# Optimization experiments

Measured on AMD Instinct MI355X. Metric: run time of the kernel, lower is better.

The kernel has to match this reference:

```python
import jax, jax.numpy as jnp
import numpy as np
from jax import lax

# ---- config (matches init_kwargs / detectron2-style inference defaults) ----
B, R, K = 8, 2000, 80          # images, proposals per image, foreground classes
H, W = 800.0, 1333.0           # image (height, width) used for box clipping
SCORE_THRESH = 0.05
NMS_THRESH = 0.5
M = 2048                        # fixed NMS candidate budget (pre-NMS top_k)
T = 100                         # topk_per_image


def setup_inputs() -> dict:
    key = jax.random.key(0)
    k1, k2, k3, k4, k5 = jax.random.split(key, 5)
    # well-formed proposal boxes (x1, y1, x2, y2)
    cx = jax.random.uniform(k1, (B, R)) * W
    cy = jax.random.uniform(k2, (B, R)) * H
    bw = jax.random.uniform(k3, (B, R)) * 300.0 + 2.0
    bh = jax.random.uniform(k4, (B, R)) * 300.0 + 2.0
    boxes = jnp.stack([cx - bw / 2, cy - bh / 2, cx + bw / 2, cy + bh / 2], axis=-1)
    k5a, k5b = jax.random.split(k5)
    scores = jax.random.uniform(k5a, (B, R, K + 1))          # (R, K+1), last col = bg
    bases = jax.random.normal(k5b, (B, R, 7)) * 0.1          # 6 base deltas + 1 h delta
    return {"boxes": boxes.astype(jnp.float32),
            "scores": scores.astype(jnp.float32),
            "bases": bases.astype(jnp.float32)}


def _delta_to_bases(bs, bx):
    # bs: (T, 6) deltas, bx: (T, 4) boxes -> (T, 10) polygon + midpoint
    firstx, firsty = bs[:, 2], bs[:, 3]
    secondx, secondy = bs[:, 4], bs[:, 5]
    x1, y1, x2, y2 = bx[:, 0], bx[:, 1], bx[:, 2], bx[:, 3]
    dx = x2 - x1
    dy = y2 - y1
    midx = (x1 + x2) / 2 + bs[:, 0] * dx
    midy = (y1 + y2) / 2 + bs[:, 1] * dy
    px1 = midx + firstx * dx
    py1 = midy + firsty * dy
    px2 = midx + secondx * dx
    py2 = midy + secondy * dy
    px3 = midx - secondx * dx
    py3 = midy - secondy * dy
    px4 = midx - firstx * dx
    py4 = midy - firsty * dy
    return jnp.stack((px1, py1, px2, py2, px3, py3, px4, py4, midx, midy), axis=-1)


def _delta_to_h(dh, bx):
    dy = bx[:, 3] - bx[:, 1]
    return dy + dh * dy


def _pairwise_iou(b):
    # b: (M, 4). Only used inside a boolean comparison -> no grad path, as in torch NMS.
    x1, y1, x2, y2 = b[:, 0], b[:, 1], b[:, 2], b[:, 3]
    area = jnp.clip(x2 - x1, 0) * jnp.clip(y2 - y1, 0)
    xx1 = jnp.maximum(x1[:, None], x1[None, :])
    yy1 = jnp.maximum(y1[:, None], y1[None, :])
    xx2 = jnp.minimum(x2[:, None], x2[None, :])
    yy2 = jnp.minimum(y2[:, None], y2[None, :])
    inter = jnp.clip(xx2 - xx1, 0) * jnp.clip(yy2 - yy1, 0)
    return inter / (area[:, None] + area[None, :] - inter + 1e-7)


def _single_image(boxes, scores, bases):
    finite = jnp.all(jnp.isfinite(boxes), axis=1) & jnp.all(jnp.isfinite(scores), axis=1)
    scores_k = scores[:, :-1]                                 # drop background (R,K)
    # Boxes.clip(image_shape)
    boxes = jnp.stack([jnp.clip(boxes[:, 0], 0.0, W),
                       jnp.clip(boxes[:, 1], 0.0, H),
                       jnp.clip(boxes[:, 2], 0.0, W),
                       jnp.clip(boxes[:, 3], 0.0, H)], axis=-1)
    # score threshold -> flat (R*K) candidate list, fixed-size top_k selection
    flat = jnp.where(finite[:, None] & (scores_k > SCORE_THRESH), scores_k, -jnp.inf)
    top_scores, top_idx = lax.top_k(flat.reshape(R * K), M)   # (M,)
    box_idx = top_idx // K
    cls = top_idx % K
    cboxes = boxes[box_idx]                                   # (M,4)
    cbases = bases[box_idx]                                   # (M,7)
    valid = jnp.isfinite(top_scores)
    # batched_nms: offset boxes per class so cross-class IoU = 0
    off = (cls.astype(boxes.dtype) * (jnp.maximum(H, W) + 2.0))[:, None]
    iou = _pairwise_iou(cboxes + off)                         # (M,M)

    def body(i, st):
        keep, supp = st
        ki = valid[i] & jnp.logical_not(supp[i])
        keep = keep.at[i].set(ki)
        supp = supp | (ki & (iou[i] > NMS_THRESH))
        return keep, supp

    keep, _ = lax.fori_loop(0, M, body,
                            (jnp.zeros((M,), bool), jnp.zeros((M,), bool)))
    masked = jnp.where(keep, top_scores, -jnp.inf)
    fscores, sel = lax.top_k(masked, T)                       # keep[:topk_per_image]
    fvalid = jnp.isfinite(fscores)
    fscores = jnp.where(fvalid, fscores, 0.0)
    fboxes = cboxes[sel] * fvalid[:, None]
    fbases = cbases[sel]
    fcls = jnp.where(fvalid, cls[sel], -1)
    h = _delta_to_h(fbases[:, 6], fboxes) * fvalid            # (T,)
    dec = _delta_to_bases(fbases[:, 0:6], fboxes) * fvalid[:, None]  # (T,10)
    return dec, h, fboxes, fscores, fcls, fvalid


def reference(boxes, scores, bases):
    # returns per-image padded detections:
    # pred_bases (B,T,10), pred_h (B,T), pred_boxes (B,T,4), scores (B,T),
    # pred_classes (B,T) int, valid mask (B,T)
    return jax.vmap(_single_image)(boxes, scores, bases)
```

## Files before the change

kernel.cpp:

```cpp
#include <hip/hip_runtime.h>
#include <stdint.h>

using u64 = unsigned long long;
using u32 = unsigned;

namespace {
constexpr int RR = 2000;
constexpr int KK = 80;
constexpr int KS = 81;
constexpr int BB = 8;
constexpr int MM = 2048;
constexpr int TT = 100;
constexpr int NB = 2048;
constexpr int CAP = 4096;
constexpr int SPLIT = 50;
constexpr int RPB = RR / SPLIT;
constexpr int FPB = RPB * KS;
constexpr int V4  = FPB / 4;
constexpr int CPB = RPB * KK;
constexpr int SPLIT_H = 10;
constexpr int RPB_H = RR / SPLIT_H;
constexpr int FPB_H = RPB_H * KS;
constexpr int V4_H  = FPB_H / 4;
constexpr float WW  = 1333.0f;
constexpr float HH  = 800.0f;
constexpr float OFF = 1335.0f;
constexpr float STH = 0.05f;
constexpr float NMS = 0.5f;

constexpr size_t HIST_OFF   = 0;
constexpr size_t CNT_OFF    = 65536;
constexpr size_t ZERO_BYTES = 65568;
constexpr size_t CSTAR_OFF  = 65568;
constexpr size_t ROWOK_OFF  = 65664;
constexpr size_t CAND_OFF   = 81920;
}

__global__ __launch_bounds__(1024) void k_hist(const float* __restrict__ boxes,
                                               const float* __restrict__ scores,
                                               u32* __restrict__ hist_g,
                                               unsigned char* __restrict__ rowok_g) {
    const int b = blockIdx.x / SPLIT_H, sb = blockIdx.x % SPLIT_H, tid = threadIdx.x;
    const int r0 = sb * RPB_H;
    const float4* sv = (const float4*)(scores + (size_t)b * RR * KS + (size_t)r0 * KS);
    __shared__ u32 bad[RPB_H];
    __shared__ u32 h[NB];

    const int q0 = tid, q1 = tid + 1024, q2 = tid + 2048, q3 = tid + 3072;
    const float4 v0 = sv[q0];
    const float4 v1 = sv[q1];
    const float4 v2 = sv[q2];
    const float4 v3 = (q3 < V4_H) ? sv[q3] : make_float4(0.f, 0.f, 0.f, 0.f);

    if (tid < RPB_H) bad[tid] = 0;
    for (int i = tid; i < NB; i += 1024) h[i] = 0;
    __syncthreads();

    if (tid < RPB_H) {
        const float4 bx = ((const float4*)(boxes + (size_t)b * RR * 4))[r0 + tid];
        if (!(isfinite(bx.x) && isfinite(bx.y) && isfinite(bx.z) && isfinite(bx.w)))
            atomicOr(&bad[tid], 1u);
    }
    auto chk = [&](int q, const float4& v) {
        if (q < V4_H) {
            const int i0 = 4 * q;
            if (!isfinite(v.x)) atomicOr(&bad[(i0    ) / KS], 1u);
            if (!isfinite(v.y)) atomicOr(&bad[(i0 + 1) / KS], 1u);
            if (!isfinite(v.z)) atomicOr(&bad[(i0 + 2) / KS], 1u);
            if (!isfinite(v.w)) atomicOr(&bad[(i0 + 3) / KS], 1u);
        }
    };
    chk(q0, v0); chk(q1, v1); chk(q2, v2); chk(q3, v3);
    __syncthreads();
    if (tid < RPB_H) rowok_g[b * RR + r0 + tid] = bad[tid] ? 0 : 1;

    auto acc = [&](int idx, float s) {
        const int r_l = idx / KS, k = idx - r_l * KS;
        if (k < KK && bad[r_l] == 0 && s > STH) {
            int bk = (int)(s * (float)NB);
            bk = min(max(bk, 0), NB - 1);
            atomicAdd(&h[bk], 1u);
        }
    };
    auto accv = [&](int q, const float4& v) {
        if (q < V4_H) {
            const int i0 = 4 * q;
            acc(i0, v.x); acc(i0 + 1, v.y); acc(i0 + 2, v.z); acc(i0 + 3, v.w);
        }
    };
    accv(q0, v0); accv(q1, v1); accv(q2, v2); accv(q3, v3);
    __syncthreads();
    for (int i = tid; i < NB; i += 1024)
        if (h[i]) atomicAdd(&hist_g[b * NB + i], h[i]);
}

__global__ __launch_bounds__(256) void k_cut(const u32* __restrict__ hist_g,
                                             u32* __restrict__ cstar_g) {
    const int b = blockIdx.x, tid = threadIdx.x;
    __shared__ u32 h[NB];
    __shared__ u32 cs[256];
    __shared__ u32 cstar_s;
    for (int i = tid; i < NB; i += 256) h[i] = hist_g[b * NB + i];
    if (tid == 0) cstar_s = 0;
    __syncthreads();

    u32 loc[8];
    const int hi = NB - 1 - 8 * tid;
    u32 sum = 0;
#pragma unroll
    for (int j = 0; j < 8; ++j) { loc[j] = h[hi - j]; sum += loc[j]; }
    cs[tid] = sum;
    __syncthreads();
    for (int s = 1; s < 256; s <<= 1) {
        const u32 t = (tid >= s) ? cs[tid - s] : 0u;
        __syncthreads();
        cs[tid] += t;
        __syncthreads();
    }
    const u32 P = cs[tid], Pm1 = (tid > 0) ? cs[tid - 1] : 0u;
    if (P >= (u32)MM && Pm1 < (u32)MM) {
        u32 run = Pm1;
#pragma unroll
        for (int j = 0; j < 8; ++j) {
            run += loc[j];
            if (run >= (u32)MM) { cstar_s = (u32)(hi - j); break; }
        }
    }
    __syncthreads();
    if (tid == 0) cstar_g[b] = cstar_s;
}

__global__ __launch_bounds__(256) void k_compact(const float* __restrict__ scores,
                                                 const u32* __restrict__ cstar_g,
                                                 const unsigned char* __restrict__ rowok_g,
                                                 u64* __restrict__ cand,
                                                 u32* __restrict__ cnt_g) {
    const int b = blockIdx.x / SPLIT, sb = blockIdx.x % SPLIT, tid = threadIdx.x;
    const int r0 = sb * RPB;
    const float4* sv = (const float4*)(scores + (size_t)b * RR * KS + (size_t)r0 * KS);
    __shared__ u64 stage[CPB];
    __shared__ u32 rok[RPB];
    __shared__ u32 scnt, base_s;
    if (tid < RPB) rok[tid] = rowok_g[b * RR + r0 + tid];
    if (tid == 0) scnt = 0;
    __syncthreads();
    const u32 cstar = cstar_g[b];

    auto put = [&](int idx, float s) {
        const int r_l = idx / KS, k = idx - r_l * KS;
        if (k < KK && rok[r_l] && s > STH) {
            int bk = (int)(s * (float)NB);
            bk = min(max(bk, 0), NB - 1);
            if ((u32)bk >= cstar) {
                const u32 p = atomicAdd(&scnt, 1u);
                const u32 eg = (u32)((r0 + r_l) * KK + k);
                stage[p] = ((u64)__float_as_uint(s) << 32) | (u32)(~eg);
            }
        }
    };
#pragma unroll
    for (int it = 0; it < 4; ++it) {
        const int q = tid + it * 256;
        if (q < V4) {
            const float4 v = sv[q];
            const int i0 = 4 * q;
            put(i0, v.x); put(i0 + 1, v.y); put(i0 + 2, v.z); put(i0 + 3, v.w);
        }
    }
    __syncthreads();
    if (tid == 0) base_s = atomicAdd(&cnt_g[b], scnt);
    __syncthreads();
    const u32 base = base_s, nn = scnt;
    u64* cb = cand + (size_t)b * CAP;
    for (u32 i = tid; i < nn; i += 256) {
        const u32 pos = base + i;
        if (pos < (u32)CAP) cb[pos] = stage[i];
    }
}

__device__ __forceinline__ void cmpsw(u64& a, u64& b, bool desc) {
    const u64 mx = a > b ? a : b, mn = a > b ? b : a;
    a = desc ? mx : mn;
    b = desc ? mn : mx;
}
template <unsigned KQ, unsigned JQ>
__device__ __forceinline__ void shfl_stage(u64 (&val)[4], int lane) {
#pragma unroll
    for (int r = 0; r < 4; ++r) {
        const unsigned v = (unsigned)(r * 64 + lane);
        const u64 pv = __shfl_xor(val[r], (int)JQ, 64);
        const bool keepmax = (((v & KQ) == 0) == (((unsigned)lane & JQ) == 0));
        val[r] = keepmax ? (val[r] > pv ? val[r] : pv)
                         : (val[r] < pv ? val[r] : pv);
    }
}

__global__ __launch_bounds__(1024) void k_sort_nms(const float* __restrict__ boxes,
                                                   const float* __restrict__ bases,
                                                   const u64* __restrict__ cand,
                                                   const u32* __restrict__ cnt_g,
                                                   float* __restrict__ out) {
#pragma clang fp contract(off)
    const int b = blockIdx.x, tid = threadIdx.x;
    const int lane = tid & 63;

    __shared__ u64 gk[CAP];
    __shared__ u32 bh[NB];
    __shared__ u32 cs[256];
    __shared__ float4 kbox[TT];
    __shared__ float  karea[TT];
    __shared__ u64    kkey[TT];
    __shared__ float4 wbox[64];
    __shared__ float  warea[64];
    __shared__ int    kcnt_s;

    const u32 n = min(cnt_g[b], (u32)CAP);
    const u64* cb = cand + (size_t)b * CAP;

    u64 myk[4]; int mi[4];
#pragma unroll
    for (int t = 0; t < 4; ++t) {
        mi[t] = tid + t * 1024;
        myk[t] = (mi[t] < (int)n) ? cb[mi[t]] : 0ull;
    }
    for (int i = tid; i < NB; i += 1024) bh[i] = 0;
    if (tid == 0) kcnt_s = 0;
    __syncthreads();

#pragma unroll
    for (int t = 0; t < 4; ++t) {
        if (mi[t] < (int)n) {
            const float s = __uint_as_float((u32)(myk[t] >> 32));
            int bk = (int)(s * (float)NB);
            bk = min(max(bk, 0), NB - 1);
            atomicAdd(&bh[bk], 1u);
        }
    }
    __syncthreads();

    u32 loc[8]; int hi = 0;
    if (tid < 256) {
        hi = NB - 1 - 8 * tid;
        u32 sum = 0;
#pragma unroll
        for (int j = 0; j < 8; ++j) { loc[j] = bh[hi - j]; sum += loc[j]; }
        cs[tid] = sum;
    }
    __syncthreads();
    for (int s = 1; s < 256; s <<= 1) {
        u32 t = 0;
        if (tid < 256 && tid >= s) t = cs[tid - s];
        __syncthreads();
        if (tid < 256) cs[tid] += t;
        __syncthreads();
    }
    if (tid < 256) {
        u32 run = (tid > 0) ? cs[tid - 1] : 0u;
#pragma unroll
        for (int j = 0; j < 8; ++j) { bh[hi - j] = run; run += loc[j]; }
    }
    __syncthreads();

#pragma unroll
    for (int t = 0; t < 4; ++t) {
        if (mi[t] < (int)n) {
            const float s = __uint_as_float((u32)(myk[t] >> 32));
            int bk = (int)(s * (float)NB);
            bk = min(max(bk, 0), NB - 1);
            const u32 pos = atomicAdd(&bh[bk], 1u);
            gk[pos] = myk[t];
        }
    }
    __syncthreads();

    if (tid < 64) {
        const float* bxp = boxes + (size_t)b * RR * 4;
        int kcnt = 0;
        int e = 0, bb = NB - 1;
        while (kcnt < TT && e < (int)n && e < MM) {
            int cend = e;
            while (bb >= 0) {
                const int bend = (int)bh[bb];
                if (bend - e <= 256) { cend = bend; --bb; if (bend - e == 256) break; }
                else break;
            }
            if (cend == e) {
                cend = min(e + 256, (int)bh[bb >= 0 ? bb : 0]); --bb;
            }
            const int csz = cend - e;

            u64 val[4];
#pragma unroll
            for (int r = 0; r < 4; ++r) {
                const int v = r * 64 + lane;
                val[r] = (v < csz) ? gk[e + v] : 0ull;
            }
            shfl_stage<2, 1>(val, lane);
            shfl_stage<4, 2>(val, lane);  shfl_stage<4, 1>(val, lane);
            shfl_stage<8, 4>(val, lane);  shfl_stage<8, 2>(val, lane);  shfl_stage<8, 1>(val, lane);
            shfl_stage<16, 8>(val, lane); shfl_stage<16, 4>(val, lane);
            shfl_stage<16, 2>(val, lane); shfl_stage<16, 1>(val, lane);
            shfl_stage<32, 16>(val, lane); shfl_stage<32, 8>(val, lane);
            shfl_stage<32, 4>(val, lane);  shfl_stage<32, 2>(val, lane); shfl_stage<32, 1>(val, lane);
            shfl_stage<64, 32>(val, lane); shfl_stage<64, 16>(val, lane);
            shfl_stage<64, 8>(val, lane);  shfl_stage<64, 4>(val, lane);
            shfl_stage<64, 2>(val, lane);  shfl_stage<64, 1>(val, lane);
            cmpsw(val[0], val[1], true);   cmpsw(val[2], val[3], false);
            shfl_stage<128, 32>(val, lane); shfl_stage<128, 16>(val, lane);
            shfl_stage<128, 8>(val, lane);  shfl_stage<128, 4>(val, lane);
            shfl_stage<128, 2>(val, lane);  shfl_stage<128, 1>(val, lane);
            cmpsw(val[0], val[2], true);   cmpsw(val[1], val[3], true);
            cmpsw(val[0], val[1], true);   cmpsw(val[2], val[3], true);
            shfl_stage<256, 32>(val, lane); shfl_stage<256, 16>(val, lane);
            shfl_stage<256, 8>(val, lane);  shfl_stage<256, 4>(val, lane);
            shfl_stage<256, 2>(val, lane);  shfl_stage<256, 1>(val, lane);

#pragma unroll 1
            for (int w = 0; w < 4; ++w) {
                if (kcnt >= TT || w * 64 >= csz) break;
                const u64 key = val[w];
                const int rank = e + w * 64 + lane;
                const bool valid = (((u32)(key >> 32)) != 0u) && (rank < MM);

                float4 box; float area;
                if (valid) {
                    const u32 idx = ~(u32)key;
                    const int rr = (int)(idx / KK), cls = (int)(idx - rr * KK);
                    const float x1 = fminf(fmaxf(bxp[rr * 4 + 0], 0.f), WW);
                    const float y1 = fminf(fmaxf(bxp[rr * 4 + 1], 0.f), HH);
                    const float x2 = fminf(fmaxf(bxp[rr * 4 + 2], 0.f), WW);
                    const float y2 = fminf(fmaxf(bxp[rr * 4 + 3], 0.f), HH);
                    const float off = (float)cls * OFF;
                    const float ox1 = x1 + off, oy1 = y1 + off;
                    const float ox2 = x2 + off, oy2 = y2 + off;
                    box = make_float4(ox1, oy1, ox2, oy2);
                    area = fmaxf(ox2 - ox1, 0.f) * fmaxf(oy2 - oy1, 0.f);
                } else {
                    box = make_float4(0.f, 0.f, 0.f, 0.f);
                    area = 0.f;
                }

                bool alive = valid;
#pragma unroll 4
                for (int kk = 0; kk < kcnt; ++kk) {
                    const float4 kb = kbox[kk];
                    const float  ka = karea[kk];
                    const float xx1 = fmaxf(kb.x, box.x), yy1 = fmaxf(kb.y, box.y);
                    const float xx2 = fminf(kb.z, box.z), yy2 = fminf(kb.w, box.w);
                    const float inter = fmaxf(xx2 - xx1, 0.f) * fmaxf(yy2 - yy1, 0.f);
                    const float iou = inter / (ka + area - inter + 1e-7f);
                    if (iou > NMS) alive = false;
                }

                wbox[lane] = box;
                warea[lane] = area;
                u64 msk = 0;
#pragma unroll 4
                for (int i = 0; i < 64; ++i) {
                    const float4 ib = wbox[i];
                    const float  ia = warea[i];
                    const float xx1 = fmaxf(ib.x, box.x), yy1 = fmaxf(ib.y, box.y);
                    const float xx2 = fminf(ib.z, box.z), yy2 = fminf(ib.w, box.w);
                    const float inter = fmaxf(xx2 - xx1, 0.f) * fmaxf(yy2 - yy1, 0.f);
                    const float iou = inter / (ia + area - inter + 1e-7f);
                    msk |= (iou > NMS ? 1ull : 0ull) << i;
                }
                msk &= (lane == 0) ? 0ull : ((1ull << lane) - 1ull);

                u64 und = __ballot(alive);
                while (und != 0ull && kcnt < TT) {
                    const int l = __ffsll((long long)und) - 1;
                    if (lane == l) {
                        kbox[kcnt]  = box;
                        karea[kcnt] = area;
                        kkey[kcnt]  = key;
                    }
                    const u64 supby = __ballot(((msk >> l) & 1ull) != 0ull);
                    und &= ~(supby | (1ull << (unsigned)l));
                    ++kcnt;
                }
            }
            e = cend;
        }
        if (lane == 0) kcnt_s = kcnt;
    }
    __syncthreads();

    if (tid < TT) {
        const int t = tid;
        const float* bx = boxes + (size_t)b * RR * 4;
        const float* bs = bases + (size_t)b * RR * 7;
        float dec[10] = {0,0,0,0,0,0,0,0,0,0};
        float hval = 0.f, fb0 = 0.f, fb1 = 0.f, fb2 = 0.f, fb3 = 0.f;
        float fs = 0.f, fc = -1.f, fv = 0.f;
        if (t < kcnt_s) {
            const u64 key = kkey[t];
            fs = __uint_as_float((u32)(key >> 32));
            const u32 idx = ~(u32)key;
            const int r = idx / KK, cls = idx - r * KK;
            const float x1 = fminf(fmaxf(bx[r * 4 + 0], 0.f), WW);
            const float y1 = fminf(fmaxf(bx[r * 4 + 1], 0.f), HH);
            const float x2 = fminf(fmaxf(bx[r * 4 + 2], 0.f), WW);
            const float y2 = fminf(fmaxf(bx[r * 4 + 3], 0.f), HH);
            const float* bp = bs + (size_t)r * 7;
            const float b0 = bp[0], b1 = bp[1], b2v = bp[2], b3v = bp[3];
            const float b4 = bp[4], b5 = bp[5], dh = bp[6];
            const float dx = x2 - x1, dy = y2 - y1;
            const float midx = (x1 + x2) / 2.0f + b0 * dx;
            const float midy = (y1 + y2) / 2.0f + b1 * dy;
            dec[0] = midx + b2v * dx; dec[1] = midy + b3v * dy;
            dec[2] = midx + b4  * dx; dec[3] = midy + b5  * dy;
            dec[4] = midx - b4  * dx; dec[5] = midy - b5  * dy;
            dec[6] = midx - b2v * dx; dec[7] = midy - b3v * dy;
            dec[8] = midx; dec[9] = midy;
            hval = dy + dh * dy;
            fb0 = x1; fb1 = y1; fb2 = x2; fb3 = y2;
            fc = (float)cls; fv = 1.f;
        }
        const size_t bt = (size_t)b * TT + t;
        float* dec_o  = out;
        float* h_o    = out + (size_t)BB * TT * 10;
        float* fbox_o = h_o + (size_t)BB * TT;
        float* fsc_o  = fbox_o + (size_t)BB * TT * 4;
        float* fcls_o = fsc_o + (size_t)BB * TT;
        float* fv_o   = fcls_o + (size_t)BB * TT;
        for (int c = 0; c < 10; ++c) dec_o[bt * 10 + c] = dec[c];
        h_o[bt] = hval;
        fbox_o[bt * 4 + 0] = fb0; fbox_o[bt * 4 + 1] = fb1;
        fbox_o[bt * 4 + 2] = fb2; fbox_o[bt * 4 + 3] = fb3;
        fsc_o[bt] = fs;
        fcls_o[bt] = fc;
        fv_o[bt] = fv;
    }
}

extern "C" void kernel_launch(void* const* d_in, const int* in_sizes, int n_in,
                              void* d_out, int out_size, void* d_ws, size_t ws_size,
                              hipStream_t stream) {
    const float* boxes  = (const float*)d_in[0];
    const float* scores = (const float*)d_in[1];
    const float* bases  = (const float*)d_in[2];
    float* out = (float*)d_out;

    char* ws = (char*)d_ws;
    u32* hist_g  = (u32*)(ws + HIST_OFF);
    u32* cnt_g   = (u32*)(ws + CNT_OFF);
    u32* cstar_g = (u32*)(ws + CSTAR_OFF);
    unsigned char* rowok_g = (unsigned char*)(ws + ROWOK_OFF);
    u64* cand    = (u64*)(ws + CAND_OFF);

    hipMemsetAsync(ws, 0, ZERO_BYTES, stream);
    hipLaunchKernelGGL(k_hist,     dim3(BB * SPLIT_H), dim3(1024), 0, stream,
                       boxes, scores, hist_g, rowok_g);
    hipLaunchKernelGGL(k_cut,      dim3(BB),           dim3(256),  0, stream,
                       hist_g, cstar_g);
    hipLaunchKernelGGL(k_compact,  dim3(BB * SPLIT),   dim3(256),  0, stream,
                       scores, cstar_g, rowok_g, cand, cnt_g);
    hipLaunchKernelGGL(k_sort_nms, dim3(BB),           dim3(1024), 0, stream,
                       boxes, bases, cand, cnt_g, out);
}
```

Baseline: 113.9 us.

## Scatter candidates into bucket-sorted order during compaction, drop memset and NMS-side sort

k_hist now writes per-block histogram slabs instead of global atomics, which removes the memset. k_cut sums the slabs and computes per-bucket start offsets. k_compact recomputes row validity itself and scatters each candidate straight to its bucket position using global atomics on the offsets. The NMS kernel therefore skips its own histogram, scan and scatter, runs with 128 threads, and reads chunks directly from global memory. In exchange there is more global atomic contention per bucket, and chunk loads in NMS now come from global memory rather than LDS.

```diff
diff --git a/kernel.cpp b/kernel.cpp
--- a/kernel.cpp
+++ b/kernel.cpp
@@ -17,7 +17,6 @@
 constexpr int RPB = RR / SPLIT;
 constexpr int FPB = RPB * KS;
 constexpr int V4  = FPB / 4;
-constexpr int CPB = RPB * KK;
 constexpr int SPLIT_H = 10;
 constexpr int RPB_H = RR / SPLIT_H;
 constexpr int FPB_H = RPB_H * KS;
@@ -28,18 +27,16 @@
 constexpr float STH = 0.05f;
 constexpr float NMS = 0.5f;
 
-constexpr size_t HIST_OFF   = 0;
-constexpr size_t CNT_OFF    = 65536;
-constexpr size_t ZERO_BYTES = 65568;
-constexpr size_t CSTAR_OFF  = 65568;
-constexpr size_t ROWOK_OFF  = 65664;
-constexpr size_t CAND_OFF   = 81920;
+constexpr size_t CUR_OFF   = 0;
+constexpr size_t HSLAB_OFF = 65536;
+constexpr size_t CNT_OFF   = 720896;
+constexpr size_t CSTAR_OFF = 720928;
+constexpr size_t CAND_OFF  = 720960;
 }
 
 __global__ __launch_bounds__(1024) void k_hist(const float* __restrict__ boxes,
                                                const float* __restrict__ scores,
-                                               u32* __restrict__ hist_g,
-                                               unsigned char* __restrict__ rowok_g) {
+                                               u32* __restrict__ hslab) {
     const int b = blockIdx.x / SPLIT_H, sb = blockIdx.x % SPLIT_H, tid = threadIdx.x;
     const int r0 = sb * RPB_H;
     const float4* sv = (const float4*)(scores + (size_t)b * RR * KS + (size_t)r0 * KS);
@@ -72,7 +69,6 @@
     };
     chk(q0, v0); chk(q1, v1); chk(q2, v2); chk(q3, v3);
     __syncthreads();
-    if (tid < RPB_H) rowok_g[b * RR + r0 + tid] = bad[tid] ? 0 : 1;
 
     auto acc = [&](int idx, float s) {
         const int r_l = idx / KS, k = idx - r_l * KS;
@@ -90,18 +86,25 @@
     };
     accv(q0, v0); accv(q1, v1); accv(q2, v2); accv(q3, v3);
     __syncthreads();
-    for (int i = tid; i < NB; i += 1024)
-        if (h[i]) atomicAdd(&hist_g[b * NB + i], h[i]);
-}
-
-__global__ __launch_bounds__(256) void k_cut(const u32* __restrict__ hist_g,
+    u32* slab = hslab + (size_t)(b * SPLIT_H + sb) * NB;
+    for (int i = tid; i < NB; i += 1024) slab[i] = h[i];
+}
+
+__global__ __launch_bounds__(256) void k_cut(const u32* __restrict__ hslab,
+                                             u32* __restrict__ cur,
+                                             u32* __restrict__ cnt_g,
                                              u32* __restrict__ cstar_g) {
     const int b = blockIdx.x, tid = threadIdx.x;
     __shared__ u32 h[NB];
     __shared__ u32 cs[256];
-    __shared__ u32 cstar_s;
-    for (int i = tid; i < NB; i += 256) h[i] = hist_g[b * NB + i];
-    if (tid == 0) cstar_s = 0;
+    __shared__ u32 cstar_s, total_s;
+    for (int i = tid; i < NB; i += 256) {
+        u32 s = 0;
+        for (int sb = 0; sb < SPLIT_H; ++sb)
+            s += hslab[(size_t)(b * SPLIT_H + sb) * NB + i];
+        h[i] = s;
+    }
+    if (tid == 0) { cstar_s = 0; total_s = 0; }
     __syncthreads();
 
     u32 loc[8];
@@ -123,58 +126,83 @@
 #pragma unroll
         for (int j = 0; j < 8; ++j) {
             run += loc[j];
-            if (run >= (u32)MM) { cstar_s = (u32)(hi - j); break; }
-        }
-    }
-    __syncthreads();
-    if (tid == 0) cstar_g[b] = cstar_s;
-}
-
-__global__ __launch_bounds__(256) void k_compact(const float* __restrict__ scores,
+            if (run >= (u32)MM) { cstar_s = (u32)(hi - j); total_s = run; break; }
+        }
+    }
+    __syncthreads();
+    const u32 cstar = cstar_s;
+    const u32 total = (total_s != 0u) ? total_s : cs[255];
+    const u32 n = min(total, (u32)CAP);
+
+    {
+        u32 run = Pm1;
+        for (int i = hi; i >= hi - 7; --i) {
+            const u32 startv = run;
+            run += h[i];
+            cur[(size_t)b * NB + i] = (i >= (int)cstar) ? startv : n;
+        }
+    }
+    if (tid == 0) { cnt_g[b] = n; cstar_g[b] = cstar; }
+}
+
+__global__ __launch_bounds__(256) void k_compact(const float* __restrict__ boxes,
+                                                 const float* __restrict__ scores,
                                                  const u32* __restrict__ cstar_g,
-                                                 const unsigned char* __restrict__ rowok_g,
-                                                 u64* __restrict__ cand,
-                                                 u32* __restrict__ cnt_g) {
+                                                 u32* __restrict__ cur,
+                                                 u64* __restrict__ cand) {
     const int b = blockIdx.x / SPLIT, sb = blockIdx.x % SPLIT, tid = threadIdx.x;
     const int r0 = sb * RPB;
     const float4* sv = (const float4*)(scores + (size_t)b * RR * KS + (size_t)r0 * KS);
-    __shared__ u64 stage[CPB];
-    __shared__ u32 rok[RPB];
-    __shared__ u32 scnt, base_s;
-    if (tid < RPB) rok[tid] = rowok_g[b * RR + r0 + tid];
-    if (tid == 0) scnt = 0;
-    __syncthreads();
+    __shared__ u32 bad[RPB];
+
+    float4 v[4]; int q[4];
+#pragma unroll
+    for (int it = 0; it < 4; ++it) {
+        q[it] = tid + it * 256;
+        if (q[it] < V4) v[it] = sv[q[it]];
+    }
+    if (tid < RPB) bad[tid] = 0;
+    __syncthreads();
+
+    if (tid < RPB) {
+        const float4 bx = ((const float4*)(boxes + (size_t)b * RR * 4))[r0 + tid];
+        if (!(isfinite(bx.x) && isfinite(bx.y) && isfinite(bx.z) && isfinite(bx.w)))
+            atomicOr(&bad[tid], 1u);
+    }
+#pragma unroll
+    for (int it = 0; it < 4; ++it) {
+        if (q[it] < V4) {
+            const float* e = (const float*)&v[it];
+            for (int j = 0; j < 4; ++j)
+                if (!isfinite(e[j])) atomicOr(&bad[(4 * q[it] + j) / KS], 1u);
+        }
+    }
+    __syncthreads();
+
     const u32 cstar = cstar_g[b];
-
+    u32* curb = cur + (size_t)b * NB;
+    u64* cb   = cand + (size_t)b * CAP;
     auto put = [&](int idx, float s) {
         const int r_l = idx / KS, k = idx - r_l * KS;
-        if (k < KK && rok[r_l] && s > STH) {
+        if (k < KK && bad[r_l] == 0 && s > STH) {
             int bk = (int)(s * (float)NB);
             bk = min(max(bk, 0), NB - 1);
             if ((u32)bk >= cstar) {
-                const u32 p = atomicAdd(&scnt, 1u);
-                const u32 eg = (u32)((r0 + r_l) * KK + k);
-                stage[p] = ((u64)__float_as_uint(s) << 32) | (u32)(~eg);
+                const u32 pos = atomicAdd(&curb[bk], 1u);
+                if (pos < (u32)CAP) {
+                    const u32 eg = (u32)((r0 + r_l) * KK + k);
+                    cb[pos] = ((u64)__float_as_uint(s) << 32) | (u32)(~eg);
+                }
             }
         }
     };
 #pragma unroll
     for (int it = 0; it < 4; ++it) {
-        const int q = tid + it * 256;
-        if (q < V4) {
-            const float4 v = sv[q];
-            const int i0 = 4 * q;
-            put(i0, v.x); put(i0 + 1, v.y); put(i0 + 2, v.z); put(i0 + 3, v.w);
-        }
-    }
-    __syncthreads();
-    if (tid == 0) base_s = atomicAdd(&cnt_g[b], scnt);
-    __syncthreads();
-    const u32 base = base_s, nn = scnt;
-    u64* cb = cand + (size_t)b * CAP;
-    for (u32 i = tid; i < nn; i += 256) {
-        const u32 pos = base + i;
-        if (pos < (u32)CAP) cb[pos] = stage[i];
+        if (q[it] < V4) {
+            const float* e = (const float*)&v[it];
+            const int i0 = 4 * q[it];
+            put(i0, e[0]); put(i0 + 1, e[1]); put(i0 + 2, e[2]); put(i0 + 3, e[3]);
+        }
     }
 }
 
@@ -195,18 +223,17 @@
     }
 }
 
-__global__ __launch_bounds__(1024) void k_sort_nms(const float* __restrict__ boxes,
-                                                   const float* __restrict__ bases,
-                                                   const u64* __restrict__ cand,
-                                                   const u32* __restrict__ cnt_g,
-                                                   float* __restrict__ out) {
+__global__ __launch_bounds__(128) void k_nms(const float* __restrict__ boxes,
+                                             const float* __restrict__ bases,
+                                             const u64* __restrict__ cand,
+                                             const u32* __restrict__ cur,
+                                             const u32* __restrict__ cnt_g,
+                                             float* __restrict__ out) {
 #pragma clang fp contract(off)
     const int b = blockIdx.x, tid = threadIdx.x;
     const int lane = tid & 63;
 
-    __shared__ u64 gk[CAP];
     __shared__ u32 bh[NB];
-    __shared__ u32 cs[256];
     __shared__ float4 kbox[TT];
     __shared__ float  karea[TT];
     __shared__ u64    kkey[TT];
@@ -214,63 +241,11 @@
     __shared__ float  warea[64];
     __shared__ int    kcnt_s;
 
-    const u32 n = min(cnt_g[b], (u32)CAP);
+    const u32 n = cnt_g[b];
     const u64* cb = cand + (size_t)b * CAP;
-
-    u64 myk[4]; int mi[4];
-#pragma unroll
-    for (int t = 0; t < 4; ++t) {
-        mi[t] = tid + t * 1024;
-        myk[t] = (mi[t] < (int)n) ? cb[mi[t]] : 0ull;
-    }
-    for (int i = tid; i < NB; i += 1024) bh[i] = 0;
+    for (int i = tid; i < NB; i += 128)
+        bh[i] = min(cur[(size_t)b * NB + i], n);
     if (tid == 0) kcnt_s = 0;
-    __syncthreads();
-
-#pragma unroll
-    for (int t = 0; t < 4; ++t) {
-        if (mi[t] < (int)n) {
-            const float s = __uint_as_float((u32)(myk[t] >> 32));
-            int bk = (int)(s * (float)NB);
-            bk = min(max(bk, 0), NB - 1);
-            atomicAdd(&bh[bk], 1u);
-        }
-    }
-    __syncthreads();
-
-    u32 loc[8]; int hi = 0;
-    if (tid < 256) {
-        hi = NB - 1 - 8 * tid;
-        u32 sum = 0;
-#pragma unroll
-        for (int j = 0; j < 8; ++j) { loc[j] = bh[hi - j]; sum += loc[j]; }
-        cs[tid] = sum;
-    }
-    __syncthreads();
-    for (int s = 1; s < 256; s <<= 1) {
-        u32 t = 0;
-        if (tid < 256 && tid >= s) t = cs[tid - s];
-        __syncthreads();
-        if (tid < 256) cs[tid] += t;
-        __syncthreads();
-    }
-    if (tid < 256) {
-        u32 run = (tid > 0) ? cs[tid - 1] : 0u;
-#pragma unroll
-        for (int j = 0; j < 8; ++j) { bh[hi - j] = run; run += loc[j]; }
-    }
-    __syncthreads();
-
-#pragma unroll
-    for (int t = 0; t < 4; ++t) {
-        if (mi[t] < (int)n) {
-            const float s = __uint_as_float((u32)(myk[t] >> 32));
-            int bk = (int)(s * (float)NB);
-            bk = min(max(bk, 0), NB - 1);
-            const u32 pos = atomicAdd(&bh[bk], 1u);
-            gk[pos] = myk[t];
-        }
-    }
     __syncthreads();
 
     if (tid < 64) {
@@ -293,7 +268,7 @@
 #pragma unroll
             for (int r = 0; r < 4; ++r) {
                 const int v = r * 64 + lane;
-                val[r] = (v < csz) ? gk[e + v] : 0ull;
+                val[r] = (v < csz) ? cb[e + v] : 0ull;
             }
             shfl_stage<2, 1>(val, lane);
             shfl_stage<4, 2>(val, lane);  shfl_stage<4, 1>(val, lane);
@@ -443,19 +418,18 @@
     float* out = (float*)d_out;
 
     char* ws = (char*)d_ws;
-    u32* hist_g  = (u32*)(ws + HIST_OFF);
+    u32* cur     = (u32*)(ws + CUR_OFF);
+    u32* hslab   = (u32*)(ws + HSLAB_OFF);
     u32* cnt_g   = (u32*)(ws + CNT_OFF);
     u32* cstar_g = (u32*)(ws + CSTAR_OFF);
-    unsigned char* rowok_g = (unsigned char*)(ws + ROWOK_OFF);
     u64* cand    = (u64*)(ws + CAND_OFF);
 
-    hipMemsetAsync(ws, 0, ZERO_BYTES, stream);
-    hipLaunchKernelGGL(k_hist,     dim3(BB * SPLIT_H), dim3(1024), 0, stream,
-                       boxes, scores, hist_g, rowok_g);
-    hipLaunchKernelGGL(k_cut,      dim3(BB),           dim3(256),  0, stream,
-                       hist_g, cstar_g);
-    hipLaunchKernelGGL(k_compact,  dim3(BB * SPLIT),   dim3(256),  0, stream,
-                       scores, cstar_g, rowok_g, cand, cnt_g);
-    hipLaunchKernelGGL(k_sort_nms, dim3(BB),           dim3(1024), 0, stream,
-                       boxes, bases, cand, cnt_g, out);
-}
+    hipLaunchKernelGGL(k_hist,    dim3(BB * SPLIT_H), dim3(1024), 0, stream,
+                       boxes, scores, hslab);
+    hipLaunchKernelGGL(k_cut,     dim3(BB),           dim3(256),  0, stream,
+                       hslab, cur, cnt_g, cstar_g);
+    hipLaunchKernelGGL(k_compact, dim3(BB * SPLIT),   dim3(256),  0, stream,
+                       boxes, scores, cstar_g, cur, cand);
+    hipLaunchKernelGGL(k_nms,     dim3(BB),           dim3(128),  0, stream,
+                       boxes, bases, cand, cur, cnt_g, out);
+}
```

After: 123.0 us. +8.0%, slower.
